# Kernel optimization log

Measured on AMD Instinct MI355X. Metric: run time of the kernel, lower is better.

Reference implementation:

```python
import jax, jax.numpy as jnp
import numpy as np

B, S_X, S_Y = 2, 2048, 2048
C1, C2, H, D, W_EXP = 1024, 1024, 16, 64, 4
EPS = 1e-5


def _layernorm(x, w, b):
    mu = jnp.mean(x, axis=-1, keepdims=True)
    var = jnp.mean(jnp.square(x - mu), axis=-1, keepdims=True)
    return (x - mu) * jax.lax.rsqrt(var + EPS) * w + b


def setup_inputs() -> dict:
    key = jax.random.key(0)
    ks = jax.random.split(key, 12)
    s = lambda fan_in: 1.0 / np.sqrt(fan_in)
    inp = {
        "x": jax.random.normal(ks[0], (B, S_X, C1), jnp.float32),
        "y": jax.random.normal(ks[1], (B, S_Y, C2), jnp.float32),
        # per-head projections, batched over heads: [H, in, d]
        "Wq": jax.random.uniform(ks[2], (H, C1, D), jnp.float32, -s(C1), s(C1)),
        "Wk": jax.random.uniform(ks[3], (H, C2, D), jnp.float32, -s(C2), s(C2)),
        "Wv": jax.random.uniform(ks[4], (H, C2, D), jnp.float32, -s(C2), s(C2)),
        "li1_w": jax.random.uniform(ks[5], (H * D, C1), jnp.float32, -s(H * D), s(H * D)),
        "li1_b": jax.random.uniform(ks[6], (C1,), jnp.float32, -s(H * D), s(H * D)),
        "ln1_w": jnp.ones((C1,), jnp.float32),
        "ln1_b": jnp.zeros((C1,), jnp.float32),
        "ln2_w": jnp.ones((C2,), jnp.float32),
        "ln2_b": jnp.zeros((C2,), jnp.float32),
        "ln3_w": jnp.ones((C1,), jnp.float32),
        "ln3_b": jnp.zeros((C1,), jnp.float32),
        "li2_w": jax.random.uniform(ks[7], (C1, C1 * W_EXP), jnp.float32, -s(C1), s(C1)),
        "li2_b": jax.random.uniform(ks[8], (C1 * W_EXP,), jnp.float32, -s(C1), s(C1)),
        "li3_w": jax.random.uniform(ks[9], (C1 * W_EXP, C1), jnp.float32, -s(C1 * W_EXP), s(C1 * W_EXP)),
        "li3_b": jax.random.uniform(ks[10], (C1,), jnp.float32, -s(C1 * W_EXP), s(C1 * W_EXP)),
    }
    return inp


def reference(x, y, Wq, Wk, Wv, li1_w, li1_b, ln1_w, ln1_b, ln2_w, ln2_b,
              ln3_w, ln3_b, li2_w, li2_b, li3_w, li3_b):
    xn = _layernorm(x, ln1_w, ln1_b)            # [B, Sx, C1]
    yn = _layernorm(y, ln2_w, ln2_b)            # [B, Sy, C2]
    # batched per-head projections (original loops over 16 Head modules)
    q = jnp.einsum("bsc,hcd->bhsd", xn, Wq)
    k = jnp.einsum("btc,hcd->bhtd", yn, Wk)
    v = jnp.einsum("btc,hcd->bhtd", yn, Wv)
    a = jnp.einsum("bhsd,bhtd->bhst", q, k) * (D ** -0.5)
    a = jax.nn.softmax(a, axis=-1)
    # faithful to original: triu(diagonal=1) applied AFTER softmax (zeros diag too)
    mask = jnp.triu(jnp.ones((S_X, S_Y), bool), k=1)
    a = jnp.where(mask, a, 0.0)
    o = jnp.einsum("bhst,bhtd->bhsd", a, v)     # [B, H, Sx, D]
    o = o.transpose(0, 2, 1, 3).reshape(B, S_X, H * D)  # concat heads
    x_out = x + o @ li1_w + li1_b
    h = _layernorm(x_out, ln3_w, ln3_b)
    h = jax.nn.gelu(h @ li2_w + li2_b, approximate=False)
    h = h @ li3_w + li3_b
    return x_out + h
```

## Files before the change

kernel.cpp:

```cpp
#include <hip/hip_runtime.h>
#include <hip/hip_bf16.h>


typedef __hip_bfloat16 bf16;
typedef __attribute__((ext_vector_type(8))) short  s16x8;
typedef __attribute__((ext_vector_type(4))) short  s16x4;
typedef __attribute__((ext_vector_type(4))) float  f32x4;
typedef __attribute__((ext_vector_type(4))) _Float16 h16x4;

__device__ __forceinline__ float bfbits2f(short s) {
    return __uint_as_float(((unsigned)(unsigned short)s) << 16);
}
__device__ __forceinline__ float load_in(const void* p, size_t i, int f32) {
    return f32 ? ((const float*)p)[i] : bfbits2f(((const short*)p)[i]);
}
__device__ __forceinline__ void async16(const short* g, short* l) {
    __builtin_amdgcn_global_load_lds(
        (const __attribute__((address_space(1))) void*)g,
        (__attribute__((address_space(3))) void*)l, 16, 0, 0);
}

__global__ __launch_bounds__(256)
void detect_dtype(const short* __restrict__ x, int* __restrict__ flag)
{
    const int tid = threadIdx.x;
    int cnt = 0;
#pragma unroll
    for (int e = 0; e < 16; e++) {
        int idx = (tid * 16 + e) * 2;
        int ex  = (x[idx] >> 7) & 0xFF;
        if (ex >= 113 && ex <= 142) cnt++;
    }
#pragma unroll
    for (int off = 1; off < 64; off <<= 1) cnt += __shfl_xor(cnt, off, 64);
    __shared__ int sh[4];
    if ((tid & 63) == 0) sh[tid >> 6] = cnt;
    __syncthreads();
    if (tid == 0) {
        int tot = sh[0] + sh[1] + sh[2] + sh[3];
        flag[0] = (tot < 2458) ? 1 : 0;
    }
}

__global__ __launch_bounds__(256)
void conv_to_bf16(const void* __restrict__ in, bf16* __restrict__ out, int n,
                  const int* __restrict__ flag)
{
    int i = (blockIdx.x * 256 + threadIdx.x) * 4;
    if (i >= n) return;
    if (flag[0]) {
        f32x4 v = *(const f32x4*)((const float*)in + i);
#pragma unroll
        for (int e = 0; e < 4; e++) out[i + e] = __float2bfloat16(v[e]);
    } else {
        *(s16x4*)((short*)out + i) = *(const s16x4*)((const short*)in + i);
    }
}

__global__ __launch_bounds__(256)
void transpose_tiled(const void* __restrict__ in, bf16* __restrict__ out,
                     int R, int Cc, const int* __restrict__ flag)
{
    __shared__ float tile[32][33];
    const int f32 = flag[0];
    const int tx = threadIdx.x & 31, ty = threadIdx.x >> 5;
    const int c0 = blockIdx.x * 32, r0 = blockIdx.y * 32;
#pragma unroll
    for (int i = 0; i < 4; i++)
        tile[ty + i * 8][tx] = load_in(in, (size_t)(r0 + ty + i * 8) * Cc + c0 + tx, f32);
    __syncthreads();
#pragma unroll
    for (int i = 0; i < 4; i++)
        out[(size_t)(c0 + ty + i * 8) * R + r0 + tx] = __float2bfloat16(tile[tx][ty + i * 8]);
}

__global__ __launch_bounds__(256)
void pack_qkv_tiled(const void* __restrict__ in, bf16* __restrict__ out,
                    const int* __restrict__ flag)
{
    __shared__ float tile[32][33];
    const int f32 = flag[0];
    const int tx = threadIdx.x & 31, ty = threadIdx.x >> 5;
    const int c0 = blockIdx.x * 32, r0 = blockIdx.y * 32;
    const size_t base = (size_t)blockIdx.z * 1024 * 64;
#pragma unroll
    for (int i = 0; i < 4; i++)
        tile[ty + i * 8][tx] = load_in(in, base + (size_t)(r0 + ty + i * 8) * 64 + c0 + tx, f32);
    __syncthreads();
#pragma unroll
    for (int i = 0; i < 4; i++)
        out[base + (size_t)(c0 + ty + i * 8) * 1024 + r0 + tx] =
            __float2bfloat16(tile[tx][ty + i * 8]);
}

__global__ __launch_bounds__(256)
void ln_kernel(const void* __restrict__ x, const void* __restrict__ w,
               const void* __restrict__ bv, bf16* __restrict__ out,
               const int* __restrict__ flag, int x_is_bf16)
{
    const int f32  = flag[0];
    const int xf32 = x_is_bf16 ? 0 : f32;
    const int row  = blockIdx.x;
    const int tid  = threadIdx.x;
    const int lane = tid & 63;
    const int wave = tid >> 6;
    const size_t base = (size_t)row * 1024 + tid * 4;

    float v[4];
    float sum = 0.f, ss = 0.f;
#pragma unroll
    for (int e = 0; e < 4; e++) {
        v[e] = load_in(x, base + e, xf32);
        sum += v[e]; ss += v[e] * v[e];
    }
#pragma unroll
    for (int off = 1; off < 64; off <<= 1) {
        sum += __shfl_xor(sum, off, 64);
        ss  += __shfl_xor(ss,  off, 64);
    }
    __shared__ float sh1[4], sh2[4];
    if (lane == 0) { sh1[wave] = sum; sh2[wave] = ss; }
    __syncthreads();
    float t1 = sh1[0] + sh1[1] + sh1[2] + sh1[3];
    float t2 = sh2[0] + sh2[1] + sh2[2] + sh2[3];
    float mu   = t1 * (1.f / 1024.f);
    float var  = t2 * (1.f / 1024.f) - mu * mu;
    float rstd = rsqrtf(var + 1e-5f);

#pragma unroll
    for (int e = 0; e < 4; e++) {
        float ov = (v[e] - mu) * rstd * load_in(w, tid * 4 + e, f32)
                 + load_in(bv, tid * 4 + e, f32);
        out[base + e] = __float2bfloat16(ov);
    }
}

template<int BN>
__global__ __launch_bounds__(256)
void gemm_bt(const bf16* __restrict__ A, const bf16* __restrict__ Bt,
             const bf16* __restrict__ bias, const bf16* __restrict__ res,
             void* __restrict__ C, int M, int N, int K, int act,
             const int* __restrict__ dflag, int final_out)
{
    constexpr int JN = BN / 32;
    __shared__ alignas(16) short As[128][32];
    __shared__ alignas(16) short Bs[BN][32];

    const int f32out = final_out ? dflag[0] : 0;
    const int tid  = threadIdx.x;
    const int lane = tid & 63;
    const int wave = tid >> 6;
    const int q    = lane >> 4;
    const int l15  = lane & 15;
    const int wm   = (wave >> 1) * 64;
    const int wn   = (wave & 1) * (BN / 2);
    const int bm   = blockIdx.x * 128;
    const int bn   = blockIdx.y * BN;

    const int lr = lane >> 2;
    const int lc = (lane & 3) * 8;

    f32x4 acc[4][JN] = {};

    const short* Abase = (const short*)A  + (size_t)(bm + wave * 32 + lr) * K + lc;
    const short* Bbase;
    if (BN == 128) Bbase = (const short*)Bt + (size_t)(bn + wave * 32 + lr) * K + lc;
    else           Bbase = (const short*)Bt + (size_t)(bn + wave * 16 + lr) * K + lc;

    for (int k0 = 0; k0 < K; k0 += 32) {
        __syncthreads();
        async16(Abase + k0,                &As[wave * 32][0]);
        async16(Abase + k0 + (size_t)16 * K, &As[wave * 32 + 16][0]);
        if (BN == 128) {
            async16(Bbase + k0,                &Bs[wave * 32][0]);
            async16(Bbase + k0 + (size_t)16 * K, &Bs[wave * 32 + 16][0]);
        } else {
            async16(Bbase + k0, &Bs[wave * 16][0]);
        }
        __syncthreads();

        s16x8 af[4], bfrag[JN];
#pragma unroll
        for (int i = 0; i < 4; i++)  af[i]    = *(const s16x8*)&As[wm + i * 16 + l15][q * 8];
#pragma unroll
        for (int j = 0; j < JN; j++) bfrag[j] = *(const s16x8*)&Bs[wn + j * 16 + l15][q * 8];
#pragma unroll
        for (int i = 0; i < 4; i++)
#pragma unroll
            for (int j = 0; j < JN; j++)
                acc[i][j] = __builtin_amdgcn_mfma_f32_16x16x32_bf16(af[i], bfrag[j], acc[i][j], 0, 0, 0);
    }

#pragma unroll
    for (int i = 0; i < 4; i++) {
#pragma unroll
        for (int j = 0; j < JN; j++) {
            int n = bn + wn + j * 16 + l15;
            float bvv = bias ? __bfloat162float(bias[n]) : 0.f;
#pragma unroll
            for (int r = 0; r < 4; r++) {
                int m = bm + wm + i * 16 + q * 4 + r;
                float v = acc[i][j][r] + bvv;
                if (act) v = 0.5f * v * (1.f + erff(v * 0.70710678118f));
                if (res) v += __bfloat162float(res[(size_t)m * N + n]);
                size_t idx = (size_t)m * N + n;
                if (f32out) ((float*)C)[idx] = v;
                else        ((bf16*)C)[idx]  = __float2bfloat16(v);
            }
        }
    }
}

__global__ __launch_bounds__(256)
void attn_kernel(const bf16* __restrict__ Q, const bf16* __restrict__ KV,
                 bf16* __restrict__ O)
{
    __shared__ alignas(16) short    Ks[64][72];
    __shared__ alignas(16) _Float16 Vs[64][72];

    const int tid  = threadIdx.x;
    const int lane = tid & 63;
    const int wave = tid >> 6;
    const int q    = lane >> 4;
    const int l15  = lane & 15;
    const int bh   = blockIdx.y;
    const int b    = bh >> 4, h = bh & 15;
    const int sblk   = blockIdx.x * 64;
    const int s_base = sblk + wave * 16;
    const int s_glob = s_base + l15;

    const short* qrow = (const short*)Q + (size_t)(b * 2048 + s_glob) * 1024 + h * 64;
    s16x8 qf0 = *(const s16x8*)(qrow + q * 8);
    s16x8 qf1 = *(const s16x8*)(qrow + 32 + q * 8);

    float l_lane = 0.f;
    f32x4 o_acc[4] = {};

    const int trow   = tid >> 2;
    const int tchunk = tid & 3;
    const int kswz   = (tchunk ^ (trow >> 2)) & 3;
    const int vcol   = (((trow >> 4) ^ tchunk) & 3) * 16 + (trow & 15);
    const int ksw    = l15 >> 2;

    for (int t0 = 0; t0 < 2048; t0 += 64) {
        const bool needV = (t0 >= sblk);
        const short* krow = (const short*)KV + (size_t)(b * 2048 + t0 + trow) * 2048 + h * 64;
        s16x8 k0 = *(const s16x8*)(krow + tchunk * 16);
        s16x8 k1 = *(const s16x8*)(krow + tchunk * 16 + 8);
        s16x8 v0, v1;
        if (needV) {
            const short* vrow = krow + 1024;
            v0 = *(const s16x8*)(vrow + tchunk * 16);
            v1 = *(const s16x8*)(vrow + tchunk * 16 + 8);
        }
        __syncthreads();
        *(s16x8*)&Ks[trow][kswz * 16]     = k0;
        *(s16x8*)&Ks[trow][kswz * 16 + 8] = k1;
        if (needV) {
#pragma unroll
            for (int e = 0; e < 8; e++) {
                Vs[tchunk * 16 + e][vcol]     = (_Float16)bfbits2f(v0[e]);
                Vs[tchunk * 16 + 8 + e][vcol] = (_Float16)bfbits2f(v1[e]);
            }
        }
        __syncthreads();

#pragma unroll
        for (int sub = 0; sub < 4; sub++) {
            const int tb  = sub * 16;
            const int rel = t0 + tb - s_base;
            s16x8 kf0 = *(const s16x8*)&Ks[tb + l15][(((q >> 1) ^ ksw) & 3) * 16 + (q & 1) * 8];
            s16x8 kf1 = *(const s16x8*)&Ks[tb + l15][((((q >> 1) + 2) ^ ksw) & 3) * 16 + (q & 1) * 8];
            f32x4 st = {};
            st = __builtin_amdgcn_mfma_f32_16x16x32_bf16(kf0, qf0, st, 0, 0, 0);
            st = __builtin_amdgcn_mfma_f32_16x16x32_bf16(kf1, qf1, st, 0, 0, 0);
            float p[4];
#pragma unroll
            for (int r = 0; r < 4; r++) {
                float sc = st[r] * 0.125f;
                p[r] = __expf(fminf(sc, 60.f));
                l_lane += p[r];
            }
            if (rel >= 0) {
                h16x4 pf;
                if (rel == 0) {
#pragma unroll
                    for (int r = 0; r < 4; r++)
                        pf[r] = (q * 4 + r > l15) ? (_Float16)p[r] : (_Float16)0.f;
                } else {
#pragma unroll
                    for (int r = 0; r < 4; r++) pf[r] = (_Float16)p[r];
                }
#pragma unroll
                for (int dt = 0; dt < 4; dt++) {
                    h16x4 vf = *(const h16x4*)&Vs[dt * 16 + l15]
                                                 [(((tb >> 4) ^ dt) & 3) * 16 + q * 4];
                    o_acc[dt] = __builtin_amdgcn_mfma_f32_16x16x16f16(pf, vf, o_acc[dt], 0, 0, 0);
                }
            }
        }
    }

    float l = l_lane;
    l += __shfl_xor(l, 16, 64);
    l += __shfl_xor(l, 32, 64);
    float linv[4];
#pragma unroll
    for (int r = 0; r < 4; r++) linv[r] = 1.f / __shfl(l, q * 4 + r, 64);
#pragma unroll
    for (int dt = 0; dt < 4; dt++)
#pragma unroll
        for (int r = 0; r < 4; r++) {
            int s = s_base + q * 4 + r;
            int d = dt * 16 + l15;
            O[(size_t)(b * 2048 + s) * 1024 + h * 64 + d] =
                __float2bfloat16(o_acc[dt][r] * linv[r]);
        }
}

extern "C" void kernel_launch(void* const* d_in, const int* in_sizes, int n_in,
                              void* d_out, int out_size, void* d_ws, size_t ws_size,
                              hipStream_t stream)
{
    const void* x     = d_in[0];
    const void* y     = d_in[1];
    const void* Wq    = d_in[2];
    const void* Wk    = d_in[3];
    const void* Wv    = d_in[4];
    const void* li1_w = d_in[5];
    const void* li1_b = d_in[6];
    const void* ln1_w = d_in[7];
    const void* ln1_b = d_in[8];
    const void* ln2_w = d_in[9];
    const void* ln2_b = d_in[10];
    const void* ln3_w = d_in[11];
    const void* ln3_b = d_in[12];
    const void* li2_w = d_in[13];
    const void* li2_b = d_in[14];
    const void* li3_w = d_in[15];
    const void* li3_b = d_in[16];

    char* w = (char*)d_ws;
    const size_t MB = 1u << 20;
    bf16* xn    = (bf16*)(w + 0 * MB);
    bf16* yn    = (bf16*)(w + 8 * MB);
    bf16* WqT   = (bf16*)(w + 16 * MB);
    bf16* WkT   = (bf16*)(w + 18 * MB);
    bf16* WvT   = (bf16*)(w + 20 * MB);
    bf16* li1T  = (bf16*)(w + 22 * MB);
    bf16* li2T  = (bf16*)(w + 24 * MB);
    bf16* li3T  = (bf16*)(w + 32 * MB);
    bf16* xout  = (bf16*)(w + 40 * MB);
    bf16* Qb    = (bf16*)(w + 48 * MB);
    bf16* KVb   = (bf16*)(w + 56 * MB);
    bf16* h2    = (bf16*)(w + 48 * MB);
    bf16* xc    = (bf16*)(w + 80 * MB);
    int*  flag  = (int*) (w + 88 * MB);
    bf16* li1bc = (bf16*)(w + 88 * MB + 4096);
    bf16* li2bc = (bf16*)(w + 88 * MB + 8192);
    bf16* li3bc = (bf16*)(w + 88 * MB + 24576);
    bf16* Ob    = yn;
    bf16* hn    = xn;

    detect_dtype<<<1, 256, 0, stream>>>((const short*)x, flag);

    conv_to_bf16<<<4096, 256, 0, stream>>>(x, xc, 4194304, flag);
    conv_to_bf16<<<1, 256, 0, stream>>>(li1_b, li1bc, 1024, flag);
    conv_to_bf16<<<4, 256, 0, stream>>>(li2_b, li2bc, 4096, flag);
    conv_to_bf16<<<1, 256, 0, stream>>>(li3_b, li3bc, 1024, flag);

    ln_kernel<<<4096, 256, 0, stream>>>(x, ln1_w, ln1_b, xn, flag, 0);
    ln_kernel<<<4096, 256, 0, stream>>>(y, ln2_w, ln2_b, yn, flag, 0);

    pack_qkv_tiled<<<dim3(2, 32, 16), 256, 0, stream>>>(Wq, WqT, flag);
    pack_qkv_tiled<<<dim3(2, 32, 16), 256, 0, stream>>>(Wk, WkT, flag);
    pack_qkv_tiled<<<dim3(2, 32, 16), 256, 0, stream>>>(Wv, WvT, flag);
    transpose_tiled<<<dim3(32, 32),  256, 0, stream>>>(li1_w, li1T, 1024, 1024, flag);
    transpose_tiled<<<dim3(128, 32), 256, 0, stream>>>(li2_w, li2T, 1024, 4096, flag);
    transpose_tiled<<<dim3(32, 128), 256, 0, stream>>>(li3_w, li3T, 4096, 1024, flag);

    gemm_bt<64><<<dim3(32, 16), 256, 0, stream>>>(xn, WqT, nullptr, nullptr, Qb, 4096, 1024, 1024, 0, flag, 0);
    gemm_bt<64><<<dim3(32, 32), 256, 0, stream>>>(yn, WkT, nullptr, nullptr, KVb, 4096, 2048, 1024, 0, flag, 0);

    attn_kernel<<<dim3(32, 32), 256, 0, stream>>>(Qb, KVb, Ob);

    gemm_bt<64><<<dim3(32, 16), 256, 0, stream>>>(Ob, li1T, li1bc, xc, xout, 4096, 1024, 1024, 0, flag, 0);

    ln_kernel<<<4096, 256, 0, stream>>>(xout, ln3_w, ln3_b, hn, flag, 1);

    gemm_bt<128><<<dim3(32, 32), 256, 0, stream>>>(hn, li2T, li2bc, nullptr, h2, 4096, 4096, 1024, 1, flag, 0);

    gemm_bt<64><<<dim3(32, 16), 256, 0, stream>>>(h2, li3T, li3bc, xout, d_out, 4096, 1024, 4096, 0, flag, 1);
}
```

Measured before the change: 543.1 us.

## Add swizzled K=64 GEMM kernel, fold x conversion into layernorm, merge bias conversions

```diff
diff --git a/kernel.cpp b/kernel.cpp
--- a/kernel.cpp
+++ b/kernel.cpp
@@ -43,18 +43,14 @@
 }
 
 __global__ __launch_bounds__(256)
-void conv_to_bf16(const void* __restrict__ in, bf16* __restrict__ out, int n,
-                  const int* __restrict__ flag)
-{
-    int i = (blockIdx.x * 256 + threadIdx.x) * 4;
-    if (i >= n) return;
-    if (flag[0]) {
-        f32x4 v = *(const f32x4*)((const float*)in + i);
-#pragma unroll
-        for (int e = 0; e < 4; e++) out[i + e] = __float2bfloat16(v[e]);
-    } else {
-        *(s16x4*)((short*)out + i) = *(const s16x4*)((const short*)in + i);
-    }
+void conv_bias3(const void* b1, const void* b2, const void* b3,
+                bf16* o1, bf16* o2, bf16* o3, const int* __restrict__ flag)
+{
+    const int f32 = flag[0];
+    int i = blockIdx.x * 256 + threadIdx.x;
+    if (i < 1024)      o1[i]        = __float2bfloat16(load_in(b1, i, f32));
+    else if (i < 5120) o2[i - 1024] = __float2bfloat16(load_in(b2, i - 1024, f32));
+    else               o3[i - 5120] = __float2bfloat16(load_in(b3, i - 5120, f32));
 }
 
 __global__ __launch_bounds__(256)
@@ -96,7 +92,8 @@
 __global__ __launch_bounds__(256)
 void ln_kernel(const void* __restrict__ x, const void* __restrict__ w,
                const void* __restrict__ bv, bf16* __restrict__ out,
-               const int* __restrict__ flag, int x_is_bf16)
+               const int* __restrict__ flag, int x_is_bf16,
+               bf16* __restrict__ copy_out)
 {
     const int f32  = flag[0];
     const int xf32 = x_is_bf16 ? 0 : f32;
@@ -112,6 +109,15 @@
     for (int e = 0; e < 4; e++) {
         v[e] = load_in(x, base + e, xf32);
         sum += v[e]; ss += v[e] * v[e];
+    }
+    if (copy_out) {
+        s16x4 c;
+#pragma unroll
+        for (int e = 0; e < 4; e++) {
+            __hip_bfloat16 hb = __float2bfloat16(v[e]);
+            c[e] = *(short*)&hb;
+        }
+        *(s16x4*)((short*)copy_out + base) = c;
     }
 #pragma unroll
     for (int off = 1; off < 64; off <<= 1) {
@@ -169,10 +175,10 @@
 
     for (int k0 = 0; k0 < K; k0 += 32) {
         __syncthreads();
-        async16(Abase + k0,                &As[wave * 32][0]);
+        async16(Abase + k0,                  &As[wave * 32][0]);
         async16(Abase + k0 + (size_t)16 * K, &As[wave * 32 + 16][0]);
         if (BN == 128) {
-            async16(Bbase + k0,                &Bs[wave * 32][0]);
+            async16(Bbase + k0,                  &Bs[wave * 32][0]);
             async16(Bbase + k0 + (size_t)16 * K, &Bs[wave * 32 + 16][0]);
         } else {
             async16(Bbase + k0, &Bs[wave * 16][0]);
@@ -195,6 +201,84 @@
     for (int i = 0; i < 4; i++) {
 #pragma unroll
         for (int j = 0; j < JN; j++) {
+            int n = bn + wn + j * 16 + l15;
+            float bvv = bias ? __bfloat162float(bias[n]) : 0.f;
+#pragma unroll
+            for (int r = 0; r < 4; r++) {
+                int m = bm + wm + i * 16 + q * 4 + r;
+                float v = acc[i][j][r] + bvv;
+                if (act) v = 0.5f * v * (1.f + erff(v * 0.70710678118f));
+                if (res) v += __bfloat162float(res[(size_t)m * N + n]);
+                size_t idx = (size_t)m * N + n;
+                if (f32out) ((float*)C)[idx] = v;
+                else        ((bf16*)C)[idx]  = __float2bfloat16(v);
+            }
+        }
+    }
+}
+
+__global__ __launch_bounds__(256)
+void gemm_bt64(const bf16* __restrict__ A, const bf16* __restrict__ Bt,
+               const bf16* __restrict__ bias, const bf16* __restrict__ res,
+               void* __restrict__ C, int M, int N, int K, int act,
+               const int* __restrict__ dflag, int final_out)
+{
+    __shared__ alignas(16) short As[128][64];
+    __shared__ alignas(16) short Bs[64][64];
+
+    const int f32out = final_out ? dflag[0] : 0;
+    const int tid  = threadIdx.x;
+    const int lane = tid & 63;
+    const int wave = tid >> 6;
+    const int q    = lane >> 4;
+    const int l15  = lane & 15;
+    const int wm   = (wave >> 1) * 64;
+    const int wn   = (wave & 1) * 32;
+    const int bm   = blockIdx.x * 128;
+    const int bn   = blockIdx.y * 64;
+
+    const int srow   = lane >> 3;
+    const int gchunk = (lane & 7) ^ srow;
+    const short* Ab = (const short*)A  + (size_t)(bm + wave * 32 + srow) * K + gchunk * 8;
+    const short* Bb = (const short*)Bt + (size_t)(bn + wave * 16 + srow) * K + gchunk * 8;
+    const int csw = l15 & 7;
+
+    f32x4 acc[4][2] = {};
+
+    for (int k0 = 0; k0 < K; k0 += 64) {
+        __syncthreads();
+        async16(Ab + k0,                  &As[wave * 32][0]);
+        async16(Ab + k0 + (size_t)8  * K, &As[wave * 32 + 8][0]);
+        async16(Ab + k0 + (size_t)16 * K, &As[wave * 32 + 16][0]);
+        async16(Ab + k0 + (size_t)24 * K, &As[wave * 32 + 24][0]);
+        async16(Bb + k0,                  &Bs[wave * 16][0]);
+        async16(Bb + k0 + (size_t)8  * K, &Bs[wave * 16 + 8][0]);
+        __syncthreads();
+
+        s16x8 af[4][2], bfr[2][2];
+#pragma unroll
+        for (int i = 0; i < 4; i++)
+#pragma unroll
+            for (int kk = 0; kk < 2; kk++)
+                af[i][kk] = *(const s16x8*)&As[wm + i * 16 + l15][((kk * 4 + q) ^ csw) * 8];
+#pragma unroll
+        for (int j = 0; j < 2; j++)
+#pragma unroll
+            for (int kk = 0; kk < 2; kk++)
+                bfr[j][kk] = *(const s16x8*)&Bs[wn + j * 16 + l15][((kk * 4 + q) ^ csw) * 8];
+#pragma unroll
+        for (int i = 0; i < 4; i++)
+#pragma unroll
+            for (int j = 0; j < 2; j++) {
+                acc[i][j] = __builtin_amdgcn_mfma_f32_16x16x32_bf16(af[i][0], bfr[j][0], acc[i][j], 0, 0, 0);
+                acc[i][j] = __builtin_amdgcn_mfma_f32_16x16x32_bf16(af[i][1], bfr[j][1], acc[i][j], 0, 0, 0);
+            }
+    }
+
+#pragma unroll
+    for (int i = 0; i < 4; i++) {
+#pragma unroll
+        for (int j = 0; j < 2; j++) {
             int n = bn + wn + j * 16 + l15;
             float bvv = bias ? __bfloat162float(bias[n]) : 0.f;
 #pragma unroll
@@ -364,13 +448,10 @@
 
     detect_dtype<<<1, 256, 0, stream>>>((const short*)x, flag);
 
-    conv_to_bf16<<<4096, 256, 0, stream>>>(x, xc, 4194304, flag);
-    conv_to_bf16<<<1, 256, 0, stream>>>(li1_b, li1bc, 1024, flag);
-    conv_to_bf16<<<4, 256, 0, stream>>>(li2_b, li2bc, 4096, flag);
-    conv_to_bf16<<<1, 256, 0, stream>>>(li3_b, li3bc, 1024, flag);
-
-    ln_kernel<<<4096, 256, 0, stream>>>(x, ln1_w, ln1_b, xn, flag, 0);
-    ln_kernel<<<4096, 256, 0, stream>>>(y, ln2_w, ln2_b, yn, flag, 0);
+    conv_bias3<<<24, 256, 0, stream>>>(li1_b, li2_b, li3_b, li1bc, li2bc, li3bc, flag);
+
+    ln_kernel<<<4096, 256, 0, stream>>>(x, ln1_w, ln1_b, xn, flag, 0, xc);
+    ln_kernel<<<4096, 256, 0, stream>>>(y, ln2_w, ln2_b, yn, flag, 0, nullptr);
 
     pack_qkv_tiled<<<dim3(2, 32, 16), 256, 0, stream>>>(Wq, WqT, flag);
     pack_qkv_tiled<<<dim3(2, 32, 16), 256, 0, stream>>>(Wk, WkT, flag);
@@ -379,16 +460,16 @@
     transpose_tiled<<<dim3(128, 32), 256, 0, stream>>>(li2_w, li2T, 1024, 4096, flag);
     transpose_tiled<<<dim3(32, 128), 256, 0, stream>>>(li3_w, li3T, 4096, 1024, flag);
 
-    gemm_bt<64><<<dim3(32, 16), 256, 0, stream>>>(xn, WqT, nullptr, nullptr, Qb, 4096, 1024, 1024, 0, flag, 0);
-    gemm_bt<64><<<dim3(32, 32), 256, 0, stream>>>(yn, WkT, nullptr, nullptr, KVb, 4096, 2048, 1024, 0, flag, 0);
+    gemm_bt64<<<dim3(32, 16), 256, 0, stream>>>(xn, WqT, nullptr, nullptr, Qb, 4096, 1024, 1024, 0, flag, 0);
+    gemm_bt64<<<dim3(32, 32), 256, 0, stream>>>(yn, WkT, nullptr, nullptr, KVb, 4096, 2048, 1024, 0, flag, 0);
 
     attn_kernel<<<dim3(32, 32), 256, 0, stream>>>(Qb, KVb, Ob);
 
-    gemm_bt<64><<<dim3(32, 16), 256, 0, stream>>>(Ob, li1T, li1bc, xc, xout, 4096, 1024, 1024, 0, flag, 0);
-
-    ln_kernel<<<4096, 256, 0, stream>>>(xout, ln3_w, ln3_b, hn, flag, 1);
+    gemm_bt64<<<dim3(32, 16), 256, 0, stream>>>(Ob, li1T, li1bc, xc, xout, 4096, 1024, 1024, 0, flag, 0);
+
+    ln_kernel<<<4096, 256, 0, stream>>>(xout, ln3_w, ln3_b, hn, flag, 1, nullptr);
 
     gemm_bt<128><<<dim3(32, 32), 256, 0, stream>>>(hn, li2T, li2bc, nullptr, h2, 4096, 4096, 1024, 1, flag, 0);
 
-    gemm_bt<64><<<dim3(32, 16), 256, 0, stream>>>(h2, li3T, li3bc, xout, d_out, 4096, 1024, 4096, 0, flag, 1);
-}
+    gemm_bt64<<<dim3(32, 16), 256, 0, stream>>>(h2, li3T, li3bc, xout, d_out, 4096, 1024, 4096, 0, flag, 1);
+}
```

Result: faster. 524.6 us (-3.4%).
